# Optimization experiments

Hardware: AMD Instinct MI355X
Metric: run time of the kernel (lower is better)

Reference implementation:

```python
import jax, jax.numpy as jnp
import numpy as np

S, D, A, H, C = 2048, 256, 64, 8, 64  # seq_len, node_dim, num_aux, num_heads, num_channels
QUAT = 4
N_TYPES = 3  # nodes, aux, rot


def _linear_params(key, out_dim, in_dim, use_bias=True):
    kw, kb = jax.random.split(key)
    lim = 1.0 / np.sqrt(in_dim)
    W = jax.random.uniform(kw, (out_dim, in_dim), minval=-lim, maxval=lim, dtype=jnp.float32)
    if not use_bias:
        return W, None
    b = jax.random.uniform(kb, (out_dim,), minval=-lim, maxval=lim, dtype=jnp.float32)
    return W, b


def setup_inputs() -> dict:
    key = jax.random.key(0)
    ks = jax.random.split(key, 8)
    nodes = jax.random.normal(ks[0], (S, D), dtype=jnp.float32)
    aux = jax.random.normal(ks[1], (S, A), dtype=jnp.float32)
    rot = jax.random.normal(ks[2], (S, QUAT), dtype=jnp.float32)
    W_nodes, b_nodes = _linear_params(ks[3], H * C * 2, D)
    W_aux, b_aux = _linear_params(ks[4], H * C * 2, A)
    W_rot, _ = _linear_params(ks[5], H * C * 2, QUAT, use_bias=False)
    W_val, b_val = _linear_params(ks[6], D * H * N_TYPES, D)
    return {
        "nodes": nodes, "aux": aux, "rot": rot,
        "W_nodes": W_nodes, "b_nodes": b_nodes,
        "W_aux": W_aux, "b_aux": b_aux,
        "W_rot": W_rot,
        "W_val": W_val, "b_val": b_val,
    }


def reference(nodes, aux, rot, W_nodes, b_nodes, W_aux, b_aux, W_rot, W_val, b_val):
    seq_len = nodes.shape[0]
    # values: (S, 3H, D)
    val = (nodes @ W_val.T + b_val).reshape(seq_len, N_TYPES * H, -1)
    # per-source k/q: each (S, H, C)
    nodes_k, nodes_q = jnp.split((nodes @ W_nodes.T + b_nodes).reshape(seq_len, H, -1), 2, -1)
    aux_k, aux_q = jnp.split((aux @ W_aux.T + b_aux).reshape(seq_len, H, -1), 2, -1)
    rot_k, rot_q = jnp.split((rot @ W_rot.T).reshape(seq_len, H, -1), 2, -1)
    # concat along head axis -> (S, 3H, C)
    k = jnp.concatenate([nodes_k, aux_k, rot_k], axis=-2)
    q = jnp.concatenate([nodes_q, aux_q, rot_q], axis=-2)
    # (S, S, 3H) score tensor, scaled by 1/sqrt(num_heads) as in the original
    logits = jnp.einsum('ihc,jhc->ijh', k, q) / jnp.sqrt(jnp.asarray(H, nodes.dtype))
    att = jax.nn.softmax(logits, axis=-2)  # softmax over the j (key) axis
    out = jnp.einsum('ijh,jhd->id', att, val)  # (S, D)
    return out
```

## Files before the change

kernel.cpp:

```cpp
#include <hip/hip_runtime.h>

#define S_LEN 2048
#define NHEAD 24
#define CDIM 64
#define DDIM 256

typedef _Float16 f16x8 __attribute__((ext_vector_type(8)));
typedef float f32x4 __attribute__((ext_vector_type(4)));

__device__ __forceinline__ ushort f2h(float f) {
    _Float16 h = (_Float16)f;
    return __builtin_bit_cast(ushort, h);
}
__device__ __forceinline__ uint pkh(float a, float b) {
    auto v = __builtin_amdgcn_cvt_pkrtz(a, b);
    return __builtin_bit_cast(uint, v);
}
__device__ __forceinline__ uint pk2(float a, float b) {
    return (uint)f2h(a) | ((uint)f2h(b) << 16);
}

__device__ __forceinline__ int4 cvt8(const float* __restrict__ p) {
    float4 a = *(const float4*)p;
    float4 b = *(const float4*)(p + 4);
    f16x8 h;
    h[0] = (_Float16)a.x; h[1] = (_Float16)a.y;
    h[2] = (_Float16)a.z; h[3] = (_Float16)a.w;
    h[4] = (_Float16)b.x; h[5] = (_Float16)b.y;
    h[6] = (_Float16)b.z; h[7] = (_Float16)b.w;
    return __builtin_bit_cast(int4, h);
}

#define SCALE_K 0.51006973f

__global__ __launch_bounds__(256) void prep_kernel(
    const float* __restrict__ nodes, const float* __restrict__ W_val,
    float* __restrict__ out, ushort* __restrict__ nodes16, ushort* __restrict__ Wval16)
{
    int idx = blockIdx.x * 256 + threadIdx.x;
    if (idx < 131072) {
        ((float4*)out)[idx] = float4{0.f, 0.f, 0.f, 0.f};
    } else if (idx < 196608) {
        int i = idx - 131072;
        *(int4*)&nodes16[i * 8] = cvt8(&nodes[i * 8]);
    } else {
        int i = idx - 196608;
        *(int4*)&Wval16[i * 8] = cvt8(&W_val[i * 8]);
    }
}

__global__ __launch_bounds__(256) void proj_kernel(
    const float* __restrict__ nodes, const float* __restrict__ W_nodes,
    const float* __restrict__ b_nodes,
    const float* __restrict__ aux, const float* __restrict__ W_aux,
    const float* __restrict__ b_aux,
    const float* __restrict__ rot, const float* __restrict__ W_rot,
    const ushort* __restrict__ nodes16, const ushort* __restrict__ Wval16,
    const float* __restrict__ b_val,
    ushort* __restrict__ Kbuf, ushort* __restrict__ Qbuf, ushort* __restrict__ Vt)
{
    __shared__ ushort Asub[128 * 72];
    __shared__ ushort Wsub[128 * 72];
    const int blk = blockIdx.x;
    const int tid = threadIdx.x;
    const int wave = tid >> 6, lane = tid & 63;
    const int g = lane >> 4, c = lane & 15;

    if (blk < 768) {
        const int wm = wave & 1, wn = wave >> 1;
        const int m0 = (blk / 48) * 128, n0 = (blk % 48) * 128;
        const int K = 256;

        f32x4 acc[16];
#pragma unroll
        for (int t = 0; t < 16; t++) acc[t] = f32x4{0, 0, 0, 0};

        for (int k0 = 0; k0 < K; k0 += 64) {
            __syncthreads();
#pragma unroll
            for (int q = 0; q < 4; q++) {
                int i = tid + 256 * q;
                int row = i >> 3, kc = (i & 7) * 8;
                *(int4*)&Asub[row * 72 + kc] = *(const int4*)&nodes16[(m0 + row) * K + k0 + kc];
                *(int4*)&Wsub[row * 72 + kc] = *(const int4*)&Wval16[(n0 + row) * K + k0 + kc];
            }
            __syncthreads();

            f16x8 af0[4], af1[4];
#pragma unroll
            for (int mt = 0; mt < 4; mt++) {
                const ushort* Ar = &Asub[(wm * 64 + mt * 16 + c) * 72 + g * 8];
                af0[mt] = *(const f16x8*)Ar;
                af1[mt] = *(const f16x8*)(Ar + 32);
            }
#pragma unroll
            for (int nt = 0; nt < 4; nt++) {
                const ushort* Wr = &Wsub[(wn * 64 + nt * 16 + c) * 72 + g * 8];
                f16x8 bf0 = *(const f16x8*)Wr;
                f16x8 bf1 = *(const f16x8*)(Wr + 32);
#pragma unroll
                for (int mt = 0; mt < 4; mt++) {
                    acc[mt * 4 + nt] = __builtin_amdgcn_mfma_f32_16x16x32_f16(af0[mt], bf0, acc[mt * 4 + nt], 0, 0, 0);
                    acc[mt * 4 + nt] = __builtin_amdgcn_mfma_f32_16x16x32_f16(af1[mt], bf1, acc[mt * 4 + nt], 0, 0, 0);
                }
            }
        }

#pragma unroll
        for (int nt = 0; nt < 4; nt++) {
            int n = n0 + wn * 64 + nt * 16 + c;
            float bv = b_val[n];
            int h = n >> 8, d = n & 255;
#pragma unroll
            for (int mt = 0; mt < 4; mt++) {
                int m = m0 + wm * 64 + mt * 16 + g * 4;
                f32x4 v = acc[mt * 4 + nt];
                uint2 pw;
                pw.x = pk2(v[0] + bv, v[1] + bv);
                pw.y = pk2(v[2] + bv, v[3] + bv);
                *(uint2*)&Vt[(h * DDIM + d) * S_LEN + m] = pw;
            }
        }
    } else if (blk < 1792) {
        const int sub = blk - 768;
        const float *A, *W, *b;
        int K, hbase;
        if (sub < 512) { A = nodes; W = W_nodes; b = b_nodes; K = 256; hbase = 0; }
        else           { A = aux;   W = W_aux;   b = b_aux;   K = 64;  hbase = 8; }
        const int t5 = sub & 511;
        const int m0 = (t5 >> 4) * 64, n0 = (t5 & 15) * 64;
        const int srow = tid >> 2;
        const int skk = (tid & 3) * 8;

        f32x4 acc[4] = {f32x4{0,0,0,0}, f32x4{0,0,0,0}, f32x4{0,0,0,0}, f32x4{0,0,0,0}};

        for (int k0 = 0; k0 < K; k0 += 32) {
            __syncthreads();
            *(int4*)&Asub[srow * 40 + skk] = cvt8(&A[(m0 + srow) * K + k0 + skk]);
            *(int4*)&Wsub[srow * 40 + skk] = cvt8(&W[(n0 + srow) * K + k0 + skk]);
            __syncthreads();
            f16x8 af = *(const f16x8*)&Asub[(wave * 16 + c) * 40 + g * 8];
#pragma unroll
            for (int t = 0; t < 4; t++) {
                f16x8 bf = *(const f16x8*)&Wsub[(t * 16 + c) * 40 + g * 8];
                acc[t] = __builtin_amdgcn_mfma_f32_16x16x32_f16(af, bf, acc[t], 0, 0, 0);
            }
        }

#pragma unroll
        for (int t = 0; t < 4; t++) {
            int n = n0 + t * 16 + c;
            float bv = b[n];
            int h = hbase + (n >> 7);
            int cc = n & 127;
            float sc = (cc < 64) ? SCALE_K : 1.0f;
#pragma unroll
            for (int r = 0; r < 4; r++) {
                int m = m0 + wave * 16 + g * 4 + r;
                ushort u = f2h((acc[t][r] + bv) * sc);
                if (cc < 64) Kbuf[(h * S_LEN + m) * CDIM + cc] = u;
                else         Qbuf[(h * S_LEN + m) * CDIM + cc - 64] = u;
            }
        }
    } else {
        int u = (blk - 1792) * 256 + tid;
        int i = u >> 7;
        int n8 = (u & 127) * 8;
        int cc = n8 & 127;
        float sc = (cc < 64) ? SCALE_K : 1.0f;
        float4 r = *(const float4*)&rot[i * 4];
        ushort pv[8];
#pragma unroll
        for (int q = 0; q < 8; q++) {
            float4 w = *(const float4*)&W_rot[(n8 + q) * 4];
            pv[q] = f2h((r.x * w.x + r.y * w.y + r.z * w.z + r.w * w.w) * sc);
        }
        int h = 16 + (n8 >> 7);
        int4 pkt = *(int4*)pv;
        if (cc < 64) *(int4*)&Kbuf[(h * S_LEN + i) * CDIM + cc] = pkt;
        else         *(int4*)&Qbuf[(h * S_LEN + i) * CDIM + cc - 64] = pkt;
    }
}

__global__ __launch_bounds__(256, 3) void flash_kernel(
    const ushort* __restrict__ Kbuf, const ushort* __restrict__ Qbuf,
    const ushort* __restrict__ Vt, float* __restrict__ out)
{
    __shared__ ushort Qlds[2][64 * 72];
    __shared__ ushort Plds[2][64 * 72];
    __shared__ float  Alds[2][64];
    __shared__ int    Need[2][4] __attribute__((aligned(16)));

    const int tid = threadIdx.x;
    const int wave = tid >> 6, lane = tid & 63;
    const int g = lane >> 4, c = lane & 15;
    const int lin = blockIdx.y * 32 + blockIdx.x;
    const int xcd = lin & 7;
    const int slot = lin >> 3;
    const int h = xcd * 3 + (slot >> 5);
    const int i0 = (slot & 31) * 64;
    const float THR = 8.0f;

    const ushort* Krow = &Kbuf[(h * S_LEN + i0 + wave * 16 + c) * CDIM + g * 8];
    f16x8 ka0 = *(const f16x8*)Krow;
    f16x8 ka1 = *(const f16x8*)(Krow + 32);

    const ushort* Vbase = &Vt[(h * DDIM + wave * 64 + c) * S_LEN + g * 8];
    const ushort* Qh = &Qbuf[h * S_LEN * CDIM];

    const int qr0 = tid >> 3, qc0 = (tid & 7) * 8;
    const int qr1 = qr0 + 32;

    *(int4*)&Qlds[0][qr0 * 72 + qc0] = *(const int4*)&Qh[qr0 * CDIM + qc0];
    *(int4*)&Qlds[0][qr1 * 72 + qc0] = *(const int4*)&Qh[qr1 * CDIM + qc0];
    int4 qn0 = *(const int4*)&Qh[(64 + qr0) * CDIM + qc0];
    int4 qn1 = *(const int4*)&Qh[(64 + qr1) * CDIM + qc0];

    f16x8 vf0[4], vf1[4];
#pragma unroll
    for (int u = 0; u < 4; u++) {
        const ushort* Vr = Vbase + (u * 16) * S_LEN;
        vf0[u] = *(const f16x8*)Vr;
        vf1[u] = *(const f16x8*)(Vr + 32);
    }

    f32x4 acc[16];
#pragma unroll
    for (int u = 0; u < 16; u++) acc[u] = f32x4{0, 0, 0, 0};
    float mrow = -1e30f, lrow = 0.f;

    __syncthreads();

    {
        f32x4 Sf[4];
#pragma unroll
        for (int jc = 0; jc < 4; jc++) {
            const ushort* Qr = &Qlds[0][(jc * 16 + c) * 72 + g * 8];
            f16x8 qb0 = *(const f16x8*)Qr;
            f16x8 qb1 = *(const f16x8*)(Qr + 32);
            f32x4 s = {0, 0, 0, 0};
            s = __builtin_amdgcn_mfma_f32_16x16x32_f16(qb0, ka0, s, 0, 0, 0);
            s = __builtin_amdgcn_mfma_f32_16x16x32_f16(qb1, ka1, s, 0, 0, 0);
            Sf[jc] = s;
        }
        float tm = -1e30f;
#pragma unroll
        for (int jc = 0; jc < 4; jc++)
            tm = fmaxf(tm, fmaxf(fmaxf(Sf[jc][0], Sf[jc][1]),
                                 fmaxf(Sf[jc][2], Sf[jc][3])));
        tm = fmaxf(tm, __shfl_xor(tm, 16));
        tm = fmaxf(tm, __shfl_xor(tm, 32));
        const bool need = __any(tm > mrow + THR);
        float nm, alpha;
        if (need) { nm = fmaxf(tm, mrow); alpha = exp2f(mrow - nm); }
        else      { nm = mrow; alpha = 1.0f; }
        if (lane == 0) Need[0][wave] = need ? 1 : 0;
        float rs = 0.f;
#pragma unroll
        for (int jc = 0; jc < 4; jc++) {
            float p0 = exp2f(Sf[jc][0] - nm);
            float p1 = exp2f(Sf[jc][1] - nm);
            float p2 = exp2f(Sf[jc][2] - nm);
            float p3 = exp2f(Sf[jc][3] - nm);
            rs += (p0 + p1) + (p2 + p3);
            uint2 w;
            w.x = pkh(p0, p1);
            w.y = pkh(p2, p3);
            *(uint2*)&Plds[0][(wave * 16 + c) * 72 + jc * 16 + g * 4] = w;
        }
        lrow = lrow * alpha + rs;
        mrow = nm;
        if (g == 0) Alds[0][wave * 16 + c] = alpha;
    }
    *(int4*)&Qlds[1][qr0 * 72 + qc0] = qn0;
    *(int4*)&Qlds[1][qr1 * 72 + qc0] = qn1;

    for (int t = 0; t < 31; ++t) {
        const int cur = t & 1, nxt = cur ^ 1;
        __syncthreads();

        if (t < 30) {
            qn0 = *(const int4*)&Qh[((t + 2) * 64 + qr0) * CDIM + qc0];
            qn1 = *(const int4*)&Qh[((t + 2) * 64 + qr1) * CDIM + qc0];
        }

        f32x4 Sf[4];
#pragma unroll
        for (int jc = 0; jc < 4; jc++) {
            const ushort* Qr = &Qlds[nxt][(jc * 16 + c) * 72 + g * 8];
            f16x8 qb0 = *(const f16x8*)Qr;
            f16x8 qb1 = *(const f16x8*)(Qr + 32);
            f32x4 s = {0, 0, 0, 0};
            s = __builtin_amdgcn_mfma_f32_16x16x32_f16(qb0, ka0, s, 0, 0, 0);
            s = __builtin_amdgcn_mfma_f32_16x16x32_f16(qb1, ka1, s, 0, 0, 0);
            Sf[jc] = s;
        }

        int4 nf = *(const int4*)&Need[cur][0];
        if (nf.x | nf.y | nf.z | nf.w) {
#pragma unroll
            for (int b = 0; b < 4; b++) {
                f32x4 ab = *(const f32x4*)&Alds[cur][b * 16 + g * 4];
#pragma unroll
                for (int u = 0; u < 4; u++) acc[b * 4 + u] *= ab;
            }
        }

#pragma unroll
        for (int b = 0; b < 4; b++) {
            const ushort* Pr = &Plds[cur][(b * 16 + c) * 72 + g * 8];
            f16x8 pa0 = *(const f16x8*)Pr;
            f16x8 pa1 = *(const f16x8*)(Pr + 32);
#pragma unroll
            for (int u = 0; u < 4; u++) {
                acc[b * 4 + u] = __builtin_amdgcn_mfma_f32_16x16x32_f16(pa0, vf0[u], acc[b * 4 + u], 0, 0, 0);
                acc[b * 4 + u] = __builtin_amdgcn_mfma_f32_16x16x32_f16(pa1, vf1[u], acc[b * 4 + u], 0, 0, 0);
            }
        }

#pragma unroll
        for (int u = 0; u < 4; u++) {
            const ushort* Vr = Vbase + (u * 16) * S_LEN + (t + 1) * 64;
            vf0[u] = *(const f16x8*)Vr;
            vf1[u] = *(const f16x8*)(Vr + 32);
        }

        {
            float tl = -1e30f;
#pragma unroll
            for (int jc = 0; jc < 4; jc++)
                tl = fmaxf(tl, fmaxf(fmaxf(Sf[jc][0], Sf[jc][1]),
                                     fmaxf(Sf[jc][2], Sf[jc][3])));
            const bool need = __any(tl > mrow + THR);
            float nm, alpha;
            if (need) {
                float tm = fmaxf(tl, __shfl_xor(tl, 16));
                tm = fmaxf(tm, __shfl_xor(tm, 32));
                nm = fmaxf(tm, mrow);
                alpha = exp2f(mrow - nm);
            } else { nm = mrow; alpha = 1.0f; }
            if (lane == 0) Need[nxt][wave] = need ? 1 : 0;
            float rs = 0.f;
#pragma unroll
            for (int jc = 0; jc < 4; jc++) {
                float p0 = exp2f(Sf[jc][0] - nm);
                float p1 = exp2f(Sf[jc][1] - nm);
                float p2 = exp2f(Sf[jc][2] - nm);
                float p3 = exp2f(Sf[jc][3] - nm);
                rs += (p0 + p1) + (p2 + p3);
                uint2 w;
                w.x = pkh(p0, p1);
                w.y = pkh(p2, p3);
                *(uint2*)&Plds[nxt][(wave * 16 + c) * 72 + jc * 16 + g * 4] = w;
            }
            lrow = lrow * alpha + rs;
            mrow = nm;
            if (g == 0) Alds[nxt][wave * 16 + c] = alpha;
        }

        if (t < 30) {
            *(int4*)&Qlds[cur][qr0 * 72 + qc0] = qn0;
            *(int4*)&Qlds[cur][qr1 * 72 + qc0] = qn1;
        }
    }

    __syncthreads();
    {
        int4 nf = *(const int4*)&Need[1][0];
        if (nf.x | nf.y | nf.z | nf.w) {
#pragma unroll
            for (int b = 0; b < 4; b++) {
                f32x4 ab = *(const f32x4*)&Alds[1][b * 16 + g * 4];
#pragma unroll
                for (int u = 0; u < 4; u++) acc[b * 4 + u] *= ab;
            }
        }
#pragma unroll
        for (int b = 0; b < 4; b++) {
            const ushort* Pr = &Plds[1][(b * 16 + c) * 72 + g * 8];
            f16x8 pa0 = *(const f16x8*)Pr;
            f16x8 pa1 = *(const f16x8*)(Pr + 32);
#pragma unroll
            for (int u = 0; u < 4; u++) {
                acc[b * 4 + u] = __builtin_amdgcn_mfma_f32_16x16x32_f16(pa0, vf0[u], acc[b * 4 + u], 0, 0, 0);
                acc[b * 4 + u] = __builtin_amdgcn_mfma_f32_16x16x32_f16(pa1, vf1[u], acc[b * 4 + u], 0, 0, 0);
            }
        }
    }

    lrow += __shfl_xor(lrow, 16);
    lrow += __shfl_xor(lrow, 32);

    __syncthreads();
    if (g == 0) Alds[0][wave * 16 + c] = 1.0f / lrow;
    __syncthreads();
#pragma unroll
    for (int b = 0; b < 4; b++) {
        f32x4 lb = *(const f32x4*)&Alds[0][b * 16 + g * 4];
#pragma unroll
        for (int u = 0; u < 4; u++)
#pragma unroll
            for (int r = 0; r < 4; r++) {
                int i = i0 + b * 16 + g * 4 + r;
                int d = wave * 64 + u * 16 + c;
                atomicAdd(&out[i * DDIM + d], acc[b * 4 + u][r] * lb[r]);
            }
    }
}

extern "C" void kernel_launch(void* const* d_in, const int* in_sizes, int n_in,
                              void* d_out, int out_size, void* d_ws, size_t ws_size,
                              hipStream_t stream) {
    const float *nodes = 0, *aux = 0, *rot = 0, *W_nodes = 0, *b_nodes = 0,
                *W_aux = 0, *b_aux = 0, *W_rot = 0, *W_val = 0, *b_val = 0;
    int i1024[2] = {-1, -1};
    int n1024 = 0;
    for (int i = 0; i < n_in; ++i) {
        const float* p = (const float*)d_in[i];
        switch (in_sizes[i]) {
            case 524288:  nodes   = p; break;
            case 131072:  aux     = p; break;
            case 8192:    rot     = p; break;
            case 262144:  W_nodes = p; break;
            case 65536:   W_aux   = p; break;
            case 4096:    W_rot   = p; break;
            case 1572864: W_val   = p; break;
            case 6144:    b_val   = p; break;
            case 1024:    if (n1024 < 2) i1024[n1024] = i; n1024++; break;
            default: break;
        }
    }
    if (n1024 == 2) {
        b_nodes = (const float*)d_in[i1024[0]];
        b_aux   = (const float*)d_in[i1024[1]];
    }
    if (!nodes || !aux || !rot || !W_nodes || !b_nodes || !W_aux || !b_aux ||
        !W_rot || !W_val || !b_val) {
        nodes   = (const float*)d_in[0];
        aux     = (const float*)d_in[1];
        rot     = (const float*)d_in[2];
        W_nodes = (const float*)d_in[3];
        b_nodes = (const float*)d_in[4];
        W_aux   = (const float*)d_in[5];
        b_aux   = (const float*)d_in[6];
        W_rot   = (const float*)d_in[7];
        W_val   = (const float*)d_in[8];
        b_val   = (const float*)d_in[9];
    }
    float* out = (float*)d_out;

    float*  Opad = (float*)d_ws;
    ushort* Kbuf = (ushort*)(Opad + S_LEN * DDIM);
    ushort* Qbuf = Kbuf + NHEAD * S_LEN * CDIM;
    ushort* Vt   = Qbuf + NHEAD * S_LEN * CDIM;
    ushort* nodes16 = Vt + NHEAD * DDIM * S_LEN;
    ushort* Wval16  = nodes16 + 524288;

    dim3 blk(256);
    prep_kernel<<<dim3(1536), blk, 0, stream>>>(nodes, W_val, out, nodes16, Wval16);
    proj_kernel<<<dim3(2816), blk, 0, stream>>>(
        nodes, W_nodes, b_nodes, aux, W_aux, b_aux, rot, W_rot,
        nodes16, Wval16, b_val, Kbuf, Qbuf, Vt);
    flash_kernel<<<dim3(32, NHEAD), blk, 0, stream>>>(Kbuf, Qbuf, Vt, out);
}
```

Before: 241.5 us.

## Fuse fp16 conversion into projection, widen K-step, add MFMA priority hints

Removes the separate prep kernel. The fp32 to fp16 conversion of nodes and W_val now happens inside the value-projection tile loads, and the output is zeroed with hipMemsetAsync. The K/Q projection path now uses a 64-wide K step with two MFMAs per tile, which halves its barrier count. The flash kernel wraps its MFMA sections in s_setprio raises to favour matrix issue. The trade-off is that each projection block re-reads and re-converts fp32 data, and the memset is still a separate launch.

```diff
diff --git a/kernel.cpp b/kernel.cpp
--- a/kernel.cpp
+++ b/kernel.cpp
@@ -33,30 +33,13 @@
 
 #define SCALE_K 0.51006973f
 
-__global__ __launch_bounds__(256) void prep_kernel(
-    const float* __restrict__ nodes, const float* __restrict__ W_val,
-    float* __restrict__ out, ushort* __restrict__ nodes16, ushort* __restrict__ Wval16)
-{
-    int idx = blockIdx.x * 256 + threadIdx.x;
-    if (idx < 131072) {
-        ((float4*)out)[idx] = float4{0.f, 0.f, 0.f, 0.f};
-    } else if (idx < 196608) {
-        int i = idx - 131072;
-        *(int4*)&nodes16[i * 8] = cvt8(&nodes[i * 8]);
-    } else {
-        int i = idx - 196608;
-        *(int4*)&Wval16[i * 8] = cvt8(&W_val[i * 8]);
-    }
-}
-
 __global__ __launch_bounds__(256) void proj_kernel(
     const float* __restrict__ nodes, const float* __restrict__ W_nodes,
     const float* __restrict__ b_nodes,
     const float* __restrict__ aux, const float* __restrict__ W_aux,
     const float* __restrict__ b_aux,
     const float* __restrict__ rot, const float* __restrict__ W_rot,
-    const ushort* __restrict__ nodes16, const ushort* __restrict__ Wval16,
-    const float* __restrict__ b_val,
+    const float* __restrict__ W_val, const float* __restrict__ b_val,
     ushort* __restrict__ Kbuf, ushort* __restrict__ Qbuf, ushort* __restrict__ Vt)
 {
     __shared__ ushort Asub[128 * 72];
@@ -81,8 +64,8 @@
             for (int q = 0; q < 4; q++) {
                 int i = tid + 256 * q;
                 int row = i >> 3, kc = (i & 7) * 8;
-                *(int4*)&Asub[row * 72 + kc] = *(const int4*)&nodes16[(m0 + row) * K + k0 + kc];
-                *(int4*)&Wsub[row * 72 + kc] = *(const int4*)&Wval16[(n0 + row) * K + k0 + kc];
+                *(int4*)&Asub[row * 72 + kc] = cvt8(&nodes[(m0 + row) * K + k0 + kc]);
+                *(int4*)&Wsub[row * 72 + kc] = cvt8(&W_val[(n0 + row) * K + k0 + kc]);
             }
             __syncthreads();
 
@@ -130,20 +113,27 @@
         const int t5 = sub & 511;
         const int m0 = (t5 >> 4) * 64, n0 = (t5 & 15) * 64;
         const int srow = tid >> 2;
-        const int skk = (tid & 3) * 8;
+        const int sc0 = (tid & 3) * 16;
 
         f32x4 acc[4] = {f32x4{0,0,0,0}, f32x4{0,0,0,0}, f32x4{0,0,0,0}, f32x4{0,0,0,0}};
 
-        for (int k0 = 0; k0 < K; k0 += 32) {
+        for (int k0 = 0; k0 < K; k0 += 64) {
             __syncthreads();
-            *(int4*)&Asub[srow * 40 + skk] = cvt8(&A[(m0 + srow) * K + k0 + skk]);
-            *(int4*)&Wsub[srow * 40 + skk] = cvt8(&W[(n0 + srow) * K + k0 + skk]);
+            *(int4*)&Asub[srow * 72 + sc0]     = cvt8(&A[(m0 + srow) * K + k0 + sc0]);
+            *(int4*)&Asub[srow * 72 + sc0 + 8] = cvt8(&A[(m0 + srow) * K + k0 + sc0 + 8]);
+            *(int4*)&Wsub[srow * 72 + sc0]     = cvt8(&W[(n0 + srow) * K + k0 + sc0]);
+            *(int4*)&Wsub[srow * 72 + sc0 + 8] = cvt8(&W[(n0 + srow) * K + k0 + sc0 + 8]);
             __syncthreads();
-            f16x8 af = *(const f16x8*)&Asub[(wave * 16 + c) * 40 + g * 8];
+            const ushort* Ar = &Asub[(wave * 16 + c) * 72 + g * 8];
+            f16x8 af0 = *(const f16x8*)Ar;
+            f16x8 af1 = *(const f16x8*)(Ar + 32);
 #pragma unroll
             for (int t = 0; t < 4; t++) {
-                f16x8 bf = *(const f16x8*)&Wsub[(t * 16 + c) * 40 + g * 8];
-                acc[t] = __builtin_amdgcn_mfma_f32_16x16x32_f16(af, bf, acc[t], 0, 0, 0);
+                const ushort* Wr = &Wsub[(t * 16 + c) * 72 + g * 8];
+                f16x8 bf0 = *(const f16x8*)Wr;
+                f16x8 bf1 = *(const f16x8*)(Wr + 32);
+                acc[t] = __builtin_amdgcn_mfma_f32_16x16x32_f16(af0, bf0, acc[t], 0, 0, 0);
+                acc[t] = __builtin_amdgcn_mfma_f32_16x16x32_f16(af1, bf1, acc[t], 0, 0, 0);
             }
         }
 
@@ -285,6 +275,7 @@
         }
 
         f32x4 Sf[4];
+        __builtin_amdgcn_s_setprio(1);
 #pragma unroll
         for (int jc = 0; jc < 4; jc++) {
             const ushort* Qr = &Qlds[nxt][(jc * 16 + c) * 72 + g * 8];
@@ -295,6 +286,7 @@
             s = __builtin_amdgcn_mfma_f32_16x16x32_f16(qb1, ka1, s, 0, 0, 0);
             Sf[jc] = s;
         }
+        __builtin_amdgcn_s_setprio(0);
 
         int4 nf = *(const int4*)&Need[cur][0];
         if (nf.x | nf.y | nf.z | nf.w) {
@@ -306,6 +298,7 @@
             }
         }
 
+        __builtin_amdgcn_s_setprio(1);
 #pragma unroll
         for (int b = 0; b < 4; b++) {
             const ushort* Pr = &Plds[cur][(b * 16 + c) * 72 + g * 8];
@@ -317,6 +310,7 @@
                 acc[b * 4 + u] = __builtin_amdgcn_mfma_f32_16x16x32_f16(pa1, vf1[u], acc[b * 4 + u], 0, 0, 0);
             }
         }
+        __builtin_amdgcn_s_setprio(0);
 
 #pragma unroll
         for (int u = 0; u < 4; u++) {
@@ -453,13 +447,12 @@
     ushort* Kbuf = (ushort*)(Opad + S_LEN * DDIM);
     ushort* Qbuf = Kbuf + NHEAD * S_LEN * CDIM;
     ushort* Vt   = Qbuf + NHEAD * S_LEN * CDIM;
-    ushort* nodes16 = Vt + NHEAD * DDIM * S_LEN;
-    ushort* Wval16  = nodes16 + 524288;
+
+    hipMemsetAsync(out, 0, S_LEN * DDIM * sizeof(float), stream);
 
     dim3 blk(256);
-    prep_kernel<<<dim3(1536), blk, 0, stream>>>(nodes, W_val, out, nodes16, Wval16);
     proj_kernel<<<dim3(2816), blk, 0, stream>>>(
         nodes, W_nodes, b_nodes, aux, W_aux, b_aux, rot, W_rot,
-        nodes16, Wval16, b_val, Kbuf, Qbuf, Vt);
+        W_val, b_val, Kbuf, Qbuf, Vt);
     flash_kernel<<<dim3(32, NHEAD), blk, 0, stream>>>(Kbuf, Qbuf, Vt, out);
 }
```

Result: no change. 240.8 us (-0.3%).
